# Kernel optimization log

Measured on AMD Instinct MI355X. Metric: run time of the kernel, lower is better.

The kernel has to match this reference:

```python
import jax, jax.numpy as jnp
import numpy as np

B = 2048; V = 2000; L = 20; E = 300; ENC = 128; DEC = 32; ATT = 128


def setup_inputs() -> dict:
    key = jax.random.key(0)
    ks = jax.random.split(key, 24)

    def lin(k, out_f, in_f, s=0.05):
        k1, k2 = jax.random.split(k)
        return (jax.random.normal(k1, (out_f, in_f), jnp.float32) * s,
                jax.random.normal(k2, (out_f,), jnp.float32) * s)

    d = {}
    d["grid_embedding"] = jax.random.normal(ks[0], (B, 5, 5, E), jnp.float32)
    d["grid_onehot"] = jax.random.uniform(ks[1], (B, 5, 5, 7), jnp.float32)
    d["inventory"] = jax.random.normal(ks[2], (B, 10, E), jnp.float32)
    d["goal"] = jax.random.normal(ks[3], (B, E), jnp.float32)
    d["encoded_captions"] = jax.random.randint(ks[4], (B, L), 0, V)
    d["caption_length"] = L  # uniform lengths -> batch_size_t == B each step
    d["W_embed"], d["b_embed"] = lin(ks[5], ENC, E)
    d["W_onehot"], d["b_onehot"] = lin(ks[6], ENC, 7)
    d["W_inv"], d["b_inv"] = lin(ks[7], ENC, E)
    d["W_goal"], d["b_goal"] = lin(ks[8], ENC, E)
    d["W_enc_att"], d["b_enc_att"] = lin(ks[9], ATT, ENC)
    d["W_dec_att"], d["b_dec_att"] = lin(ks[10], ATT, DEC)
    d["W_full_att"], d["b_full_att"] = lin(ks[11], 1, ATT)
    d["emb_table"] = jax.random.normal(ks[12], (V + 1, E), jnp.float32) * 0.05
    d["W_ih"], d["b_ih"] = lin(ks[13], 4 * DEC, E + ENC)  # PyTorch LSTMCell i,f,g,o
    d["W_hh"], d["b_hh"] = lin(ks[14], 4 * DEC, DEC)
    d["W_init_h"], d["b_init_h"] = lin(ks[15], DEC, ENC)
    d["W_init_c"], d["b_init_c"] = lin(ks[16], DEC, ENC)
    d["W_fbeta"], d["b_fbeta"] = lin(ks[17], ENC, DEC)
    d["W_fc"], d["b_fc"] = lin(ks[18], V, DEC)
    return d


def reference(grid_embedding, grid_onehot, inventory, goal, encoded_captions, caption_length,
              W_embed, b_embed, W_onehot, b_onehot, W_inv, b_inv, W_goal, b_goal,
              W_enc_att, b_enc_att, W_dec_att, b_dec_att, W_full_att, b_full_att,
              emb_table, W_ih, b_ih, W_hh, b_hh, W_init_h, b_init_h, W_init_c, b_init_c,
              W_fbeta, b_fbeta, W_fc, b_fc):
    relu = jax.nn.relu
    sig = jax.nn.sigmoid
    # Encoder: grid (B,5,5,*) -> (B,25,ENC); inventory -> (B,10,ENC); goal -> (B,1,ENC)
    c1 = relu(jnp.einsum('bhwe,ce->bhwc', grid_embedding, W_embed) + b_embed)
    c2 = relu(jnp.einsum('bhws,cs->bhwc', grid_onehot, W_onehot) + b_onehot)
    grid = (c1 + c2).reshape(c1.shape[0], 25, -1)
    c3 = relu(inventory @ W_inv.T + b_inv)
    c4 = relu(goal @ W_goal.T + b_goal)[:, None, :]
    enc = jnp.concatenate([grid, c3, c4], axis=1)  # (B, 36, ENC)

    mean_enc = enc.mean(axis=1)
    h = mean_enc @ W_init_h.T + b_init_h  # (B, DEC)
    c = mean_enc @ W_init_c.T + b_init_c
    att1 = enc @ W_enc_att.T + b_enc_att  # (B, 36, ATT), time-invariant, precomputed

    emb = emb_table[encoded_captions]  # (B, L, E)
    T = caption_length - 1
    xs = jnp.transpose(emb[:, :T, :], (1, 0, 2))  # (T, B, E)

    def step(carry, emb_t):
        h, c = carry
        # additive attention
        att2 = h @ W_dec_att.T + b_dec_att
        e = relu(att1 + att2[:, None, :]) @ W_full_att[0] + b_full_att[0]  # (B, 36)
        alpha = jax.nn.softmax(e, axis=1)
        awe = jnp.einsum('bpe,bp->be', enc, alpha)
        gate = sig(h @ W_fbeta.T + b_fbeta)
        x = jnp.concatenate([emb_t, gate * awe], axis=1)
        # PyTorch LSTMCell
        gates = x @ W_ih.T + b_ih + h @ W_hh.T + b_hh
        i, f, g, o = jnp.split(gates, 4, axis=1)
        c_new = sig(f) * c + sig(i) * jnp.tanh(g)
        h_new = sig(o) * jnp.tanh(c_new)
        preds = h_new @ W_fc.T + b_fc  # dropout is identity at eval
        return (h_new, c_new), (preds, alpha)

    (h, c), (preds, alphas) = jax.lax.scan(step, (h, c), xs)
    predictions = jnp.transpose(preds, (1, 0, 2))  # (B, T, V)
    alphas = jnp.transpose(alphas, (1, 0, 2))      # (B, T, 36)
    return predictions, alphas, h
```

## Files before the change

### kernel.cpp

```cpp
#include <hip/hip_runtime.h>


__device__ __forceinline__ float dot4f(float4 a, float4 b) {
  return fmaf(a.x, b.x, fmaf(a.y, b.y, fmaf(a.z, b.z, a.w * b.w)));
}
__device__ __forceinline__ float sigmf_(float x) {
  x = fminf(fmaxf(x, -30.f), 30.f);
  return 1.f / (1.f + __expf(-x));
}
__device__ __forceinline__ float tanhf_(float x) {
  x = fminf(fmaxf(x, -15.f), 15.f);
  float e = __expf(2.f * x);
  return (e - 1.f) / (e + 1.f);
}

__global__ __launch_bounds__(256, 2) void lin_gemm(
    const float* __restrict__ X, int xstride, const int* __restrict__ gather,
    const float* __restrict__ W, int K, int wstride,
    const float* __restrict__ bias,
    const float* __restrict__ X2, const float* __restrict__ W2,
    const float* __restrict__ bias2,
    float* __restrict__ Y, int omode, int relu) {
  __shared__ __align__(16) float Xs[16 * 260];
  __shared__ __align__(16) float Ws[16 * 132];
  const int tid = threadIdx.x;
  const int tc = tid & 15, tr = tid >> 4;
  const int rbase = blockIdx.x * 256;

  float acc[16][8];
#pragma unroll
  for (int i = 0; i < 16; ++i)
#pragma unroll
    for (int j = 0; j < 8; ++j) acc[i][j] = 0.f;

  for (int k0 = 0; k0 < K; k0 += 16) {
#pragma unroll
    for (int it = 0; it < 4; ++it) {
      int tsk = tid + it * 256;
      int r = tsk >> 2, kq = tsk & 3;
      int rg = rbase + r;
      const float* xrow =
          gather ? (X + (size_t)gather[(rg / 19) * 20 + (rg % 19)] * xstride)
                 : (X + (size_t)rg * xstride);
      int kk = k0 + kq * 4;
      float4 v;
      if (kk + 3 < K)
        v = *(const float4*)(xrow + kk);
      else {
        v.x = (kk + 0 < K) ? xrow[kk + 0] : 0.f;
        v.y = (kk + 1 < K) ? xrow[kk + 1] : 0.f;
        v.z = (kk + 2 < K) ? xrow[kk + 2] : 0.f;
        v.w = (kk + 3 < K) ? xrow[kk + 3] : 0.f;
      }
      Xs[(kq * 4 + 0) * 260 + r] = v.x;
      Xs[(kq * 4 + 1) * 260 + r] = v.y;
      Xs[(kq * 4 + 2) * 260 + r] = v.z;
      Xs[(kq * 4 + 3) * 260 + r] = v.w;
    }
#pragma unroll
    for (int it = 0; it < 2; ++it) {
      int tsk = tid + it * 256;
      int c = tsk >> 2, kq = tsk & 3;
      const float* wrow = W + (size_t)c * wstride;
      int kk = k0 + kq * 4;
      float4 v;
      if (kk + 3 < K)
        v = *(const float4*)(wrow + kk);
      else {
        v.x = (kk + 0 < K) ? wrow[kk + 0] : 0.f;
        v.y = (kk + 1 < K) ? wrow[kk + 1] : 0.f;
        v.z = (kk + 2 < K) ? wrow[kk + 2] : 0.f;
        v.w = (kk + 3 < K) ? wrow[kk + 3] : 0.f;
      }
      Ws[(kq * 4 + 0) * 132 + c] = v.x;
      Ws[(kq * 4 + 1) * 132 + c] = v.y;
      Ws[(kq * 4 + 2) * 132 + c] = v.z;
      Ws[(kq * 4 + 3) * 132 + c] = v.w;
    }
    __syncthreads();
#pragma unroll
    for (int kk = 0; kk < 16; ++kk) {
      const float* xp = &Xs[kk * 260 + tr * 16];
      float4 xa = *(const float4*)(xp);
      float4 xb = *(const float4*)(xp + 4);
      float4 xc = *(const float4*)(xp + 8);
      float4 xd = *(const float4*)(xp + 12);
      float4 wA = *(const float4*)&Ws[kk * 132 + tc * 4];
      float4 wB = *(const float4*)&Ws[kk * 132 + 64 + tc * 4];
      float xr[16] = {xa.x, xa.y, xa.z, xa.w, xb.x, xb.y, xb.z, xb.w,
                      xc.x, xc.y, xc.z, xc.w, xd.x, xd.y, xd.z, xd.w};
      float wr[8] = {wA.x, wA.y, wA.z, wA.w, wB.x, wB.y, wB.z, wB.w};
#pragma unroll
      for (int i = 0; i < 16; ++i)
#pragma unroll
        for (int j = 0; j < 8; ++j) acc[i][j] = fmaf(xr[i], wr[j], acc[i][j]);
    }
    __syncthreads();
  }

  float w2r[7][8];
  if (X2) {
#pragma unroll
    for (int k = 0; k < 7; ++k)
      Xs[k * 260 + tid] = X2[(size_t)(rbase + tid) * 7 + k];
#pragma unroll
    for (int it = 0; it < 4; ++it) {
      int tsk = tid + it * 256;
      int c = tsk >> 3, k = tsk & 7;
      if (k < 7) Ws[k * 132 + c] = W2[(size_t)c * 7 + k];
    }
    __syncthreads();
#pragma unroll
    for (int k = 0; k < 7; ++k) {
      float4 a = *(const float4*)&Ws[k * 132 + tc * 4];
      float4 b = *(const float4*)&Ws[k * 132 + 64 + tc * 4];
      w2r[k][0] = a.x; w2r[k][1] = a.y; w2r[k][2] = a.z; w2r[k][3] = a.w;
      w2r[k][4] = b.x; w2r[k][5] = b.y; w2r[k][6] = b.z; w2r[k][7] = b.w;
    }
  }

  float4 bA = *(const float4*)(bias + tc * 4);
  float4 bB = *(const float4*)(bias + 64 + tc * 4);
  float bq[8] = {bA.x, bA.y, bA.z, bA.w, bB.x, bB.y, bB.z, bB.w};
  float b2q[8];
  if (X2) {
    float4 cA = *(const float4*)(bias2 + tc * 4);
    float4 cB = *(const float4*)(bias2 + 64 + tc * 4);
    b2q[0] = cA.x; b2q[1] = cA.y; b2q[2] = cA.z; b2q[3] = cA.w;
    b2q[4] = cB.x; b2q[5] = cB.y; b2q[6] = cB.z; b2q[7] = cB.w;
  }

#pragma unroll
  for (int i = 0; i < 16; ++i) {
    int rg = rbase + tr * 16 + i;
    size_t orow;
    if (omode == 0)
      orow = (size_t)((rg / 25) * 36 + rg % 25) * 128;
    else if (omode == 1)
      orow = (size_t)((rg / 10) * 36 + 25 + rg % 10) * 128;
    else if (omode == 2)
      orow = (size_t)rg * 36 * 128 + 35 * 128;
    else
      orow = (size_t)rg * 128;
    float o[8];
#pragma unroll
    for (int j = 0; j < 8; ++j) {
      float v = acc[i][j] + bq[j];
      if (relu) v = fmaxf(v, 0.f);
      o[j] = v;
    }
    if (X2) {
      float a2[8];
#pragma unroll
      for (int j = 0; j < 8; ++j) a2[j] = b2q[j];
#pragma unroll
      for (int k = 0; k < 7; ++k) {
        float xv = Xs[k * 260 + tr * 16 + i];
#pragma unroll
        for (int j = 0; j < 8; ++j) a2[j] = fmaf(xv, w2r[k][j], a2[j]);
      }
#pragma unroll
      for (int j = 0; j < 8; ++j) o[j] += fmaxf(a2[j], 0.f);
    }
    *(float4*)(Y + orow + tc * 4) = make_float4(o[0], o[1], o[2], o[3]);
    *(float4*)(Y + orow + 64 + tc * 4) = make_float4(o[4], o[5], o[6], o[7]);
  }
}

__global__ void init_hc(const float* __restrict__ enc,
                        const float* __restrict__ Wh, const float* __restrict__ bh,
                        const float* __restrict__ Wc, const float* __restrict__ bc,
                        float* __restrict__ h0, float* __restrict__ c0) {
  int b = blockIdx.x, l = threadIdx.x;
  __shared__ __align__(16) float mean[128];
  float s0 = 0.f, s1 = 0.f;
  const float* e = enc + (size_t)b * 36 * 128;
  for (int p = 0; p < 36; ++p) {
    s0 += e[p * 128 + l];
    s1 += e[p * 128 + 64 + l];
  }
  mean[l] = s0 * (1.f / 36.f);
  mean[64 + l] = s1 * (1.f / 36.f);
  __syncthreads();
  int k = l & 31;
  const float* Wm = (l < 32) ? Wh : Wc;
  float a = (l < 32) ? bh[k] : bc[k];
#pragma unroll
  for (int c4 = 0; c4 < 32; ++c4) {
    float4 mq = *(const float4*)&mean[c4 * 4];
    float4 wv = *(const float4*)(Wm + (size_t)k * 128 + c4 * 4);
    a += dot4f(mq, wv);
  }
  if (l < 32)
    h0[(size_t)b * 32 + k] = a;
  else
    c0[(size_t)b * 32 + k] = a;
}

#define SLOT(w, r) (18944 + (((w) * 3 + ((r) < (w) ? (r) : (r) - 1)) << 7))

__global__ __launch_bounds__(256, 2) void recurrent_k(
    const float* __restrict__ ws_enc, const float* __restrict__ ws_att1,
    const float* __restrict__ ws_embW, const float* __restrict__ ws_h0,
    const float* __restrict__ ws_c0, const float* __restrict__ W_dec_att,
    const float* __restrict__ b_dec_att, const float* __restrict__ W_full_att,
    const float* __restrict__ W_ih, const float* __restrict__ W_hh,
    const float* __restrict__ b_hh, const float* __restrict__ W_fbeta,
    const float* __restrict__ b_fbeta, float* __restrict__ ws_H,
    float* __restrict__ out_alpha, float* __restrict__ out_h) {
  extern __shared__ float lds[];
  const int tid = threadIdx.x;
  const int wave = tid >> 6, lane = tid & 63;
  const int m = lane & 31, s = lane >> 5;
  const int b = blockIdx.x * 4 + wave;

  const int encB = wave * 4608;
  const int x2B = 18432 + wave * 128;
  const int att2B = SLOT((wave + 1) & 3, wave);
  const int ghB = SLOT((wave + 2) & 3, wave);

  float a1m[64];
  {
    const float* base = ws_att1 + ((size_t)b * 36 + m) * 128 + 64 * s;
#pragma unroll
    for (int q4 = 0; q4 < 16; ++q4) {
      float4 v = *(const float4*)(base + 4 * q4);
      a1m[4 * q4 + 0] = v.x; a1m[4 * q4 + 1] = v.y;
      a1m[4 * q4 + 2] = v.z; a1m[4 * q4 + 3] = v.w;
    }
  }
  float a1x[8];
  {
    const float* base =
        ws_att1 + ((size_t)b * 36 + 32 + (lane & 3)) * 128 + (lane >> 2) * 8;
    float4 v0 = *(const float4*)(base);
    float4 v1 = *(const float4*)(base + 4);
    a1x[0] = v0.x; a1x[1] = v0.y; a1x[2] = v0.z; a1x[3] = v0.w;
    a1x[4] = v1.x; a1x[5] = v1.y; a1x[6] = v1.z; a1x[7] = v1.w;
  }
  float wq[4][16];
#pragma unroll
  for (int j = 0; j < 4; ++j) {
    const float* base =
        W_ih + (size_t)(4 * m + j) * 428 + 300 + 32 * wave + 16 * s;
#pragma unroll
    for (int qq = 0; qq < 4; ++qq) {
      float4 v = *(const float4*)(base + 4 * qq);
      wq[j][4 * qq + 0] = v.x; wq[j][4 * qq + 1] = v.y;
      wq[j][4 * qq + 2] = v.z; wq[j][4 * qq + 3] = v.w;
    }
  }
  const float bdec0 = b_dec_att[lane], bdec1 = b_dec_att[lane + 64];
  float4 bfbq = *(const float4*)(b_fbeta + 4 * m);
  float4 bhhq = *(const float4*)(b_hh + 4 * m);
  float creg[4];
  {
    float4 cq = *(const float4*)(ws_c0 + (size_t)b * 32 + 4 * (m & 7));
    creg[0] = cq.x; creg[1] = cq.y; creg[2] = cq.z; creg[3] = cq.w;
  }

  {
    const float* src = ws_enc + (size_t)blockIdx.x * 4 * 4608;
    for (int i = tid; i < 4608; i += 256)
      *(float4*)&lds[i * 4] = *(const float4*)(src + (size_t)i * 4);
  }
  if (m < 8 && s == 0) {
    float4 hq = *(const float4*)(ws_h0 + (size_t)b * 32 + 4 * m);
    *(float4*)&lds[ghB + 4 * m] = hq;
  }
  __syncthreads();

  for (int t = 0; t < 19; ++t) {
    float at2a = bdec0, at2b = bdec1;
    float whhp0 = 0, whhp1 = 0, whhp2 = 0, whhp3 = 0;
    float gatp0 = 0, gatp1 = 0, gatp2 = 0, gatp3 = 0;
#pragma unroll
    for (int kc = 0; kc < 8; ++kc) {
      float4 hq = *(const float4*)&lds[ghB + kc * 4];
      float4 wa = *(const float4*)(W_dec_att + (size_t)lane * 32 + kc * 4);
      float4 wb = *(const float4*)(W_dec_att + (size_t)(lane + 64) * 32 + kc * 4);
      at2a += dot4f(hq, wa);
      at2b += dot4f(hq, wb);
      if ((kc >> 2) == s) {
        float4 w0 = *(const float4*)(W_hh + (size_t)(4 * m + 0) * 32 + kc * 4);
        float4 w1 = *(const float4*)(W_hh + (size_t)(4 * m + 1) * 32 + kc * 4);
        float4 w2 = *(const float4*)(W_hh + (size_t)(4 * m + 2) * 32 + kc * 4);
        float4 w3 = *(const float4*)(W_hh + (size_t)(4 * m + 3) * 32 + kc * 4);
        whhp0 += dot4f(hq, w0); whhp1 += dot4f(hq, w1);
        whhp2 += dot4f(hq, w2); whhp3 += dot4f(hq, w3);
        float4 f0 = *(const float4*)(W_fbeta + (size_t)(4 * m + 0) * 32 + kc * 4);
        float4 f1 = *(const float4*)(W_fbeta + (size_t)(4 * m + 1) * 32 + kc * 4);
        float4 f2 = *(const float4*)(W_fbeta + (size_t)(4 * m + 2) * 32 + kc * 4);
        float4 f3 = *(const float4*)(W_fbeta + (size_t)(4 * m + 3) * 32 + kc * 4);
        gatp0 += dot4f(hq, f0); gatp1 += dot4f(hq, f1);
        gatp2 += dot4f(hq, f2); gatp3 += dot4f(hq, f3);
      }
    }
    lds[att2B + lane] = at2a;
    lds[att2B + 64 + lane] = at2b;

    float ep = 0.f;
#pragma unroll
    for (int q4 = 0; q4 < 16; ++q4) {
      float4 a2v = *(const float4*)&lds[att2B + 64 * s + 4 * q4];
      float4 wfv = *(const float4*)(W_full_att + 64 * s + 4 * q4);
      ep += fmaxf(a1m[4 * q4 + 0] + a2v.x, 0.f) * wfv.x;
      ep += fmaxf(a1m[4 * q4 + 1] + a2v.y, 0.f) * wfv.y;
      ep += fmaxf(a1m[4 * q4 + 2] + a2v.z, 0.f) * wfv.z;
      ep += fmaxf(a1m[4 * q4 + 3] + a2v.w, 0.f) * wfv.w;
    }
    ep += __shfl_xor(ep, 32);
    float ex2 = 0.f;
    {
      int a0 = (lane >> 2) * 8;
      float4 xa = *(const float4*)&lds[att2B + a0];
      float4 xb = *(const float4*)&lds[att2B + a0 + 4];
      float4 fa = *(const float4*)(W_full_att + a0);
      float4 fb = *(const float4*)(W_full_att + a0 + 4);
      ex2 += fmaxf(a1x[0] + xa.x, 0.f) * fa.x;
      ex2 += fmaxf(a1x[1] + xa.y, 0.f) * fa.y;
      ex2 += fmaxf(a1x[2] + xa.z, 0.f) * fa.z;
      ex2 += fmaxf(a1x[3] + xa.w, 0.f) * fa.w;
      ex2 += fmaxf(a1x[4] + xb.x, 0.f) * fb.x;
      ex2 += fmaxf(a1x[5] + xb.y, 0.f) * fb.y;
      ex2 += fmaxf(a1x[6] + xb.z, 0.f) * fb.z;
      ex2 += fmaxf(a1x[7] + xb.w, 0.f) * fb.w;
      ex2 += __shfl_xor(ex2, 4);
      ex2 += __shfl_xor(ex2, 8);
      ex2 += __shfl_xor(ex2, 16);
      ex2 += __shfl_xor(ex2, 32);
    }
    float ev = (s == 0) ? ep : ((m < 4) ? ex2 : -1e30f);
    float mx = ev;
    mx = fmaxf(mx, __shfl_xor(mx, 1));
    mx = fmaxf(mx, __shfl_xor(mx, 2));
    mx = fmaxf(mx, __shfl_xor(mx, 4));
    mx = fmaxf(mx, __shfl_xor(mx, 8));
    mx = fmaxf(mx, __shfl_xor(mx, 16));
    mx = fmaxf(mx, __shfl_xor(mx, 32));
    float eu = __expf(ev - mx);
    float su = eu;
    su += __shfl_xor(su, 1);
    su += __shfl_xor(su, 2);
    su += __shfl_xor(su, 4);
    su += __shfl_xor(su, 8);
    su += __shfl_xor(su, 16);
    su += __shfl_xor(su, 32);
    float alpha = eu / su;
    {
      size_t ob = ((size_t)b * 19 + t) * 36;
      if (s == 0)
        out_alpha[ob + m] = alpha;
      else if (m < 4)
        out_alpha[ob + 32 + m] = alpha;
    }

    float aw0 = 0, aw1 = 0, aw2 = 0, aw3 = 0;
#pragma unroll
    for (int pp = 0; pp < 18; ++pp) {
      float al = __shfl(alpha, 18 * s + pp);
      float4 evv = *(const float4*)&lds[encB + (18 * s + pp) * 128 + 4 * m];
      aw0 += evv.x * al; aw1 += evv.y * al;
      aw2 += evv.z * al; aw3 += evv.w * al;
    }
    aw0 += __shfl_xor(aw0, 32); aw1 += __shfl_xor(aw1, 32);
    aw2 += __shfl_xor(aw2, 32); aw3 += __shfl_xor(aw3, 32);

    float g0 = gatp0 + __shfl_xor(gatp0, 32) + bfbq.x;
    float g1 = gatp1 + __shfl_xor(gatp1, 32) + bfbq.y;
    float g2 = gatp2 + __shfl_xor(gatp2, 32) + bfbq.z;
    float g3 = gatp3 + __shfl_xor(gatp3, 32) + bfbq.w;
    float x20 = sigmf_(g0) * aw0, x21 = sigmf_(g1) * aw1;
    float x22 = sigmf_(g2) * aw2, x23 = sigmf_(g3) * aw3;
    if (s == 0) *(float4*)&lds[x2B + 4 * m] = make_float4(x20, x21, x22, x23);
    __syncthreads();

    float ownE0 = 0, ownE1 = 0, ownE2 = 0, ownE3 = 0;
#pragma unroll
    for (int rr = 0; rr < 4; ++rr) {
      float p0 = 0, p1 = 0, p2 = 0, p3 = 0;
#pragma unroll
      for (int cc = 0; cc < 4; ++cc) {
        float4 xv = *(const float4*)&lds[18432 + rr * 128 + 32 * wave + 16 * s + 4 * cc];
        p0 += wq[0][4 * cc + 0] * xv.x + wq[0][4 * cc + 1] * xv.y +
              wq[0][4 * cc + 2] * xv.z + wq[0][4 * cc + 3] * xv.w;
        p1 += wq[1][4 * cc + 0] * xv.x + wq[1][4 * cc + 1] * xv.y +
              wq[1][4 * cc + 2] * xv.z + wq[1][4 * cc + 3] * xv.w;
        p2 += wq[2][4 * cc + 0] * xv.x + wq[2][4 * cc + 1] * xv.y +
              wq[2][4 * cc + 2] * xv.z + wq[2][4 * cc + 3] * xv.w;
        p3 += wq[3][4 * cc + 0] * xv.x + wq[3][4 * cc + 1] * xv.y +
              wq[3][4 * cc + 2] * xv.z + wq[3][4 * cc + 3] * xv.w;
      }
      if (rr == wave) {
        ownE0 = p0; ownE1 = p1; ownE2 = p2; ownE3 = p3;
      } else {
        p0 += __shfl_xor(p0, 32); p1 += __shfl_xor(p1, 32);
        p2 += __shfl_xor(p2, 32); p3 += __shfl_xor(p3, 32);
        if (s == 0)
          *(float4*)&lds[SLOT(wave, rr) + 4 * m] = make_float4(p0, p1, p2, p3);
      }
    }
    __syncthreads();

    float own0 = ownE0 + whhp0, own1 = ownE1 + whhp1;
    float own2 = ownE2 + whhp2, own3 = ownE3 + whhp3;
    own0 += __shfl_xor(own0, 32); own1 += __shfl_xor(own1, 32);
    own2 += __shfl_xor(own2, 32); own3 += __shfl_xor(own3, 32);
    float4 fA = *(const float4*)&lds[SLOT((wave + 1) & 3, wave) + 4 * m];
    float4 fB = *(const float4*)&lds[SLOT((wave + 2) & 3, wave) + 4 * m];
    float4 fC = *(const float4*)&lds[SLOT((wave + 3) & 3, wave) + 4 * m];
    float4 ew = *(const float4*)(ws_embW + ((size_t)b * 19 + t) * 128 + 4 * m);
    float gg0 = own0 + fA.x + fB.x + fC.x + ew.x + bhhq.x;
    float gg1 = own1 + fA.y + fB.y + fC.y + ew.y + bhhq.y;
    float gg2 = own2 + fA.z + fB.z + fC.z + ew.z + bhhq.z;
    float gg3 = own3 + fA.w + fB.w + fC.w + ew.w + bhhq.w;
    if (s == 0) *(float4*)&lds[ghB + 4 * m] = make_float4(gg0, gg1, gg2, gg3);
    if (m < 8) {
      float4 gi = *(const float4*)&lds[ghB + 4 * m];
      float4 gf = *(const float4*)&lds[ghB + 32 + 4 * m];
      float4 gG = *(const float4*)&lds[ghB + 64 + 4 * m];
      float4 go = *(const float4*)&lds[ghB + 96 + 4 * m];
      float c0n = sigmf_(gf.x) * creg[0] + sigmf_(gi.x) * tanhf_(gG.x);
      float c1n = sigmf_(gf.y) * creg[1] + sigmf_(gi.y) * tanhf_(gG.y);
      float c2n = sigmf_(gf.z) * creg[2] + sigmf_(gi.z) * tanhf_(gG.z);
      float c3n = sigmf_(gf.w) * creg[3] + sigmf_(gi.w) * tanhf_(gG.w);
      float h0n = sigmf_(go.x) * tanhf_(c0n);
      float h1n = sigmf_(go.y) * tanhf_(c1n);
      float h2n = sigmf_(go.z) * tanhf_(c2n);
      float h3n = sigmf_(go.w) * tanhf_(c3n);
      creg[0] = c0n; creg[1] = c1n; creg[2] = c2n; creg[3] = c3n;
      if (s == 0) {
        float4 hv = make_float4(h0n, h1n, h2n, h3n);
        *(float4*)&lds[ghB + 4 * m] = hv;
        *(float4*)(ws_H + ((size_t)b * 19 + t) * 32 + 4 * m) = hv;
        if (t == 18) *(float4*)(out_h + (size_t)b * 32 + 4 * m) = hv;
      }
    }
  }
}

#define FC_RB 152
#define FC_WT_ST 1026
#define FC_HS_ST 154

__global__ __launch_bounds__(512, 1) void fc_out2(const float* __restrict__ H,
                                                  const float* __restrict__ W,
                                                  const float* __restrict__ bias,
                                                  float* __restrict__ Y) {
  extern __shared__ float sm[];
  float* Wt = sm;
  float* Hs = sm + 32 * FC_WT_ST;
  const int tid = threadIdx.x;
  const int tc = tid & 127;
  const int rt = tid >> 7;
  const int rbase = blockIdx.x * FC_RB;

  for (int i = tid; i < FC_RB * 8; i += 512) {
    int r = i >> 3, kq = i & 7;
    float4 v = *(const float4*)(H + (size_t)(rbase + r) * 32 + kq * 4);
    Hs[(kq * 4 + 0) * FC_HS_ST + r] = v.x;
    Hs[(kq * 4 + 1) * FC_HS_ST + r] = v.y;
    Hs[(kq * 4 + 2) * FC_HS_ST + r] = v.z;
    Hs[(kq * 4 + 3) * FC_HS_ST + r] = v.w;
  }

  for (int ph = 0; ph < 2; ++ph) {
    const int phbase = ph * 1024;
    const int ncols = (ph == 0) ? 1024 : 976;
    __syncthreads();
    for (int c = tid; c < ncols; c += 512) {
      const float* wrow = W + (size_t)(phbase + c) * 32;
#pragma unroll
      for (int q = 0; q < 8; ++q) {
        float4 v = *(const float4*)(wrow + q * 4);
        Wt[(q * 4 + 0) * FC_WT_ST + c] = v.x;
        Wt[(q * 4 + 1) * FC_WT_ST + c] = v.y;
        Wt[(q * 4 + 2) * FC_WT_ST + c] = v.z;
        Wt[(q * 4 + 3) * FC_WT_ST + c] = v.w;
      }
    }
    __syncthreads();

    float bq[4][2];
#pragma unroll
    for (int ch = 0; ch < 4; ++ch) {
      int col = phbase + ch * 256 + 2 * tc;
      bq[ch][0] = (col < 2000) ? bias[col] : 0.f;
      bq[ch][1] = (col < 2000) ? bias[col + 1] : 0.f;
    }

    for (int pass = 0; pass < 5; ++pass) {
      int r0 = pass * 32 + rt * 8;
      if (r0 + 8 > FC_RB) continue;
      float acc[8][8];
#pragma unroll
      for (int i = 0; i < 8; ++i)
#pragma unroll
        for (int j = 0; j < 8; ++j) acc[i][j] = 0.f;
#pragma unroll 8
      for (int k = 0; k < 32; ++k) {
        float4 ha = *(const float4*)&Hs[k * FC_HS_ST + r0];
        float4 hb = *(const float4*)&Hs[k * FC_HS_ST + r0 + 4];
        float hr[8] = {ha.x, ha.y, ha.z, ha.w, hb.x, hb.y, hb.z, hb.w};
        float2 w0 = *(const float2*)&Wt[k * FC_WT_ST + 0 * 256 + 2 * tc];
        float2 w1 = *(const float2*)&Wt[k * FC_WT_ST + 1 * 256 + 2 * tc];
        float2 w2 = *(const float2*)&Wt[k * FC_WT_ST + 2 * 256 + 2 * tc];
        float2 w3 = *(const float2*)&Wt[k * FC_WT_ST + 3 * 256 + 2 * tc];
        float wc[8] = {w0.x, w0.y, w1.x, w1.y, w2.x, w2.y, w3.x, w3.y};
#pragma unroll
        for (int i = 0; i < 8; ++i)
#pragma unroll
          for (int j = 0; j < 8; ++j) acc[i][j] = fmaf(hr[i], wc[j], acc[i][j]);
      }
#pragma unroll
      for (int i = 0; i < 8; ++i) {
        size_t row = (size_t)(rbase + r0 + i);
#pragma unroll
        for (int ch = 0; ch < 4; ++ch) {
          int col = phbase + ch * 256 + 2 * tc;
          if (col < 2000) {
            float2 v;
            v.x = acc[i][2 * ch + 0] + bq[ch][0];
            v.y = acc[i][2 * ch + 1] + bq[ch][1];
            *(float2*)(Y + row * 2000 + col) = v;
          }
        }
      }
    }
  }
}

extern "C" void kernel_launch(void* const* d_in, const int* in_sizes, int n_in,
                              void* d_out, int out_size, void* d_ws,
                              size_t ws_size, hipStream_t stream) {
  (void)in_sizes; (void)n_in; (void)out_size; (void)ws_size;
  const float* grid_embedding = (const float*)d_in[0];
  const float* grid_onehot = (const float*)d_in[1];
  const float* inventory = (const float*)d_in[2];
  const float* goal = (const float*)d_in[3];
  const int* captions = (const int*)d_in[4];
  const float* W_embed = (const float*)d_in[6];
  const float* b_embed = (const float*)d_in[7];
  const float* W_onehot = (const float*)d_in[8];
  const float* b_onehot = (const float*)d_in[9];
  const float* W_inv = (const float*)d_in[10];
  const float* b_inv = (const float*)d_in[11];
  const float* W_goal = (const float*)d_in[12];
  const float* b_goal = (const float*)d_in[13];
  const float* W_enc_att = (const float*)d_in[14];
  const float* b_enc_att = (const float*)d_in[15];
  const float* W_dec_att = (const float*)d_in[16];
  const float* b_dec_att = (const float*)d_in[17];
  const float* W_full_att = (const float*)d_in[18];
  const float* emb_table = (const float*)d_in[20];
  const float* W_ih = (const float*)d_in[21];
  const float* b_ih = (const float*)d_in[22];
  const float* W_hh = (const float*)d_in[23];
  const float* b_hh = (const float*)d_in[24];
  const float* W_init_h = (const float*)d_in[25];
  const float* b_init_h = (const float*)d_in[26];
  const float* W_init_c = (const float*)d_in[27];
  const float* b_init_c = (const float*)d_in[28];
  const float* W_fbeta = (const float*)d_in[29];
  const float* b_fbeta = (const float*)d_in[30];
  const float* W_fc = (const float*)d_in[31];
  const float* b_fc = (const float*)d_in[32];

  float* out = (float*)d_out;
  float* preds = out;
  float* alphas = out + (size_t)77824000;
  float* houtp = out + (size_t)79224832;

  float* ws = (float*)d_ws;
  float* ws_enc = ws;
  float* ws_att1 = ws_enc + (size_t)9437184;
  float* ws_embW = ws_att1 + (size_t)9437184;
  float* ws_H = ws_embW + (size_t)4980736;
  float* ws_h0 = ws_H + (size_t)1245184;
  float* ws_c0 = ws_h0 + (size_t)65536;

  lin_gemm<<<200, 256, 0, stream>>>(grid_embedding, 300, nullptr, W_embed, 300,
                                    300, b_embed, grid_onehot, W_onehot,
                                    b_onehot, ws_enc, 0, 1);
  lin_gemm<<<80, 256, 0, stream>>>(inventory, 300, nullptr, W_inv, 300, 300,
                                   b_inv, nullptr, nullptr, nullptr, ws_enc, 1, 1);
  lin_gemm<<<8, 256, 0, stream>>>(goal, 300, nullptr, W_goal, 300, 300, b_goal,
                                  nullptr, nullptr, nullptr, ws_enc, 2, 1);
  init_hc<<<2048, 64, 0, stream>>>(ws_enc, W_init_h, b_init_h, W_init_c,
                                   b_init_c, ws_h0, ws_c0);
  lin_gemm<<<288, 256, 0, stream>>>(ws_enc, 128, nullptr, W_enc_att, 128, 128,
                                    b_enc_att, nullptr, nullptr, nullptr,
                                    ws_att1, 3, 0);
  lin_gemm<<<152, 256, 0, stream>>>(emb_table, 300, captions, W_ih, 300, 428,
                                    b_ih, nullptr, nullptr, nullptr, ws_embW, 3, 0);
  hipFuncSetAttribute((const void*)recurrent_k,
                      hipFuncAttributeMaxDynamicSharedMemorySize, 81920);
  recurrent_k<<<512, 256, 81920, stream>>>(
      ws_enc, ws_att1, ws_embW, ws_h0, ws_c0, W_dec_att, b_dec_att, W_full_att,
      W_ih, W_hh, b_hh, W_fbeta, b_fbeta, ws_H, alphas, houtp);
  hipFuncSetAttribute((const void*)fc_out2,
                      hipFuncAttributeMaxDynamicSharedMemorySize, 151040);
  fc_out2<<<256, 512, 151040, stream>>>(ws_H, W_fc, b_fc, preds);
}
```

Measured before the change: 1.627 ms.

## Stage recurrent weights in LDS transposed and keep encoder rows in registers

The recurrent kernel now copies W_dec_att, W_hh, W_fbeta (transposed) and W_full_att into LDS once, instead of re-reading them from global memory on every time step. Each lane keeps its two encoder columns across all 36 positions in registers (float2 x36), so the attention-weighted sum runs without LDS encoder reads or cross-half shuffles. The per-step embW load is issued at the top of the loop to hide its latency. LDS use drops from 80KB to about 57KB, but register pressure grows with 72 extra floats per lane, which could cause spills under launch_bounds(256,2).

```diff
diff --git a/kernel.cpp b/kernel.cpp
--- a/kernel.cpp
+++ b/kernel.cpp
@@ -197,7 +197,11 @@
     c0[(size_t)b * 32 + k] = a;
 }
 
-#define SLOT(w, r) (18944 + (((w) * 3 + ((r) < (w) ? (r) : (r) - 1)) << 7))
+#define RK_WHH 4096
+#define RK_WFB 8192
+#define RK_WFA 12288
+#define RK_X2 12416
+#define SLOT(w, r) (12928 + (((w) * 3 + ((r) < (w) ? (r) : (r) - 1)) << 7))
 
 __global__ __launch_bounds__(256, 2) void recurrent_k(
     const float* __restrict__ ws_enc, const float* __restrict__ ws_att1,
@@ -214,11 +218,36 @@
   const int m = lane & 31, s = lane >> 5;
   const int b = blockIdx.x * 4 + wave;
 
-  const int encB = wave * 4608;
-  const int x2B = 18432 + wave * 128;
+  const int x2B = RK_X2 + wave * 128;
   const int att2B = SLOT((wave + 1) & 3, wave);
   const int ghB = SLOT((wave + 2) & 3, wave);
 
+  for (int tsk = tid; tsk < 1024; tsk += 256) {
+    int row = tsk & 127, kq = tsk >> 7;
+    float4 vd = *(const float4*)(W_dec_att + (size_t)row * 32 + kq * 4);
+    lds[(4 * kq + 0) * 128 + row] = vd.x;
+    lds[(4 * kq + 1) * 128 + row] = vd.y;
+    lds[(4 * kq + 2) * 128 + row] = vd.z;
+    lds[(4 * kq + 3) * 128 + row] = vd.w;
+    float4 vh = *(const float4*)(W_hh + (size_t)row * 32 + kq * 4);
+    lds[RK_WHH + (4 * kq + 0) * 128 + row] = vh.x;
+    lds[RK_WHH + (4 * kq + 1) * 128 + row] = vh.y;
+    lds[RK_WHH + (4 * kq + 2) * 128 + row] = vh.z;
+    lds[RK_WHH + (4 * kq + 3) * 128 + row] = vh.w;
+    float4 vf = *(const float4*)(W_fbeta + (size_t)row * 32 + kq * 4);
+    lds[RK_WFB + (4 * kq + 0) * 128 + row] = vf.x;
+    lds[RK_WFB + (4 * kq + 1) * 128 + row] = vf.y;
+    lds[RK_WFB + (4 * kq + 2) * 128 + row] = vf.z;
+    lds[RK_WFB + (4 * kq + 3) * 128 + row] = vf.w;
+  }
+  if (tid < 128) lds[RK_WFA + tid] = W_full_att[tid];
+
+  float2 enc_r[36];
+  {
+    const float* ebase = ws_enc + (size_t)b * 4608 + 2 * lane;
+#pragma unroll
+    for (int p = 0; p < 36; ++p) enc_r[p] = *(const float2*)(ebase + p * 128);
+  }
   float a1m[64];
   {
     const float* base = ws_att1 + ((size_t)b * 36 + m) * 128 + 64 * s;
@@ -251,19 +280,13 @@
     }
   }
   const float bdec0 = b_dec_att[lane], bdec1 = b_dec_att[lane + 64];
-  float4 bfbq = *(const float4*)(b_fbeta + 4 * m);
+  const float2 bfb2 = *(const float2*)(b_fbeta + 2 * lane);
   float4 bhhq = *(const float4*)(b_hh + 4 * m);
   float creg[4];
   {
     float4 cq = *(const float4*)(ws_c0 + (size_t)b * 32 + 4 * (m & 7));
     creg[0] = cq.x; creg[1] = cq.y; creg[2] = cq.z; creg[3] = cq.w;
   }
-
-  {
-    const float* src = ws_enc + (size_t)blockIdx.x * 4 * 4608;
-    for (int i = tid; i < 4608; i += 256)
-      *(float4*)&lds[i * 4] = *(const float4*)(src + (size_t)i * 4);
-  }
   if (m < 8 && s == 0) {
     float4 hq = *(const float4*)(ws_h0 + (size_t)b * 32 + 4 * m);
     *(float4*)&lds[ghB + 4 * m] = hq;
@@ -271,30 +294,27 @@
   __syncthreads();
 
   for (int t = 0; t < 19; ++t) {
+    float4 ew = *(const float4*)(ws_embW + ((size_t)b * 19 + t) * 128 + 4 * m);
+
     float at2a = bdec0, at2b = bdec1;
+    float ga = 0.f, gb = 0.f;
+#pragma unroll
+    for (int k = 0; k < 32; ++k) {
+      float hk = lds[ghB + k];
+      at2a = fmaf(hk, lds[k * 128 + lane], at2a);
+      at2b = fmaf(hk, lds[k * 128 + 64 + lane], at2b);
+      float2 wf = *(const float2*)&lds[RK_WFB + k * 128 + 2 * lane];
+      ga = fmaf(hk, wf.x, ga);
+      gb = fmaf(hk, wf.y, gb);
+    }
     float whhp0 = 0, whhp1 = 0, whhp2 = 0, whhp3 = 0;
-    float gatp0 = 0, gatp1 = 0, gatp2 = 0, gatp3 = 0;
-#pragma unroll
-    for (int kc = 0; kc < 8; ++kc) {
-      float4 hq = *(const float4*)&lds[ghB + kc * 4];
-      float4 wa = *(const float4*)(W_dec_att + (size_t)lane * 32 + kc * 4);
-      float4 wb = *(const float4*)(W_dec_att + (size_t)(lane + 64) * 32 + kc * 4);
-      at2a += dot4f(hq, wa);
-      at2b += dot4f(hq, wb);
-      if ((kc >> 2) == s) {
-        float4 w0 = *(const float4*)(W_hh + (size_t)(4 * m + 0) * 32 + kc * 4);
-        float4 w1 = *(const float4*)(W_hh + (size_t)(4 * m + 1) * 32 + kc * 4);
-        float4 w2 = *(const float4*)(W_hh + (size_t)(4 * m + 2) * 32 + kc * 4);
-        float4 w3 = *(const float4*)(W_hh + (size_t)(4 * m + 3) * 32 + kc * 4);
-        whhp0 += dot4f(hq, w0); whhp1 += dot4f(hq, w1);
-        whhp2 += dot4f(hq, w2); whhp3 += dot4f(hq, w3);
-        float4 f0 = *(const float4*)(W_fbeta + (size_t)(4 * m + 0) * 32 + kc * 4);
-        float4 f1 = *(const float4*)(W_fbeta + (size_t)(4 * m + 1) * 32 + kc * 4);
-        float4 f2 = *(const float4*)(W_fbeta + (size_t)(4 * m + 2) * 32 + kc * 4);
-        float4 f3 = *(const float4*)(W_fbeta + (size_t)(4 * m + 3) * 32 + kc * 4);
-        gatp0 += dot4f(hq, f0); gatp1 += dot4f(hq, f1);
-        gatp2 += dot4f(hq, f2); gatp3 += dot4f(hq, f3);
-      }
+#pragma unroll
+    for (int kc = 0; kc < 16; ++kc) {
+      int k = 16 * s + kc;
+      float hk = lds[ghB + k];
+      float4 wh = *(const float4*)&lds[RK_WHH + k * 128 + 4 * m];
+      whhp0 = fmaf(hk, wh.x, whhp0); whhp1 = fmaf(hk, wh.y, whhp1);
+      whhp2 = fmaf(hk, wh.z, whhp2); whhp3 = fmaf(hk, wh.w, whhp3);
     }
     lds[att2B + lane] = at2a;
     lds[att2B + 64 + lane] = at2b;
@@ -303,7 +323,7 @@
 #pragma unroll
     for (int q4 = 0; q4 < 16; ++q4) {
       float4 a2v = *(const float4*)&lds[att2B + 64 * s + 4 * q4];
-      float4 wfv = *(const float4*)(W_full_att + 64 * s + 4 * q4);
+      float4 wfv = *(const float4*)&lds[RK_WFA + 64 * s + 4 * q4];
       ep += fmaxf(a1m[4 * q4 + 0] + a2v.x, 0.f) * wfv.x;
       ep += fmaxf(a1m[4 * q4 + 1] + a2v.y, 0.f) * wfv.y;
       ep += fmaxf(a1m[4 * q4 + 2] + a2v.z, 0.f) * wfv.z;
@@ -315,8 +335,8 @@
       int a0 = (lane >> 2) * 8;
       float4 xa = *(const float4*)&lds[att2B + a0];
       float4 xb = *(const float4*)&lds[att2B + a0 + 4];
-      float4 fa = *(const float4*)(W_full_att + a0);
-      float4 fb = *(const float4*)(W_full_att + a0 + 4);
+      float4 fa = *(const float4*)&lds[RK_WFA + a0];
+      float4 fb = *(const float4*)&lds[RK_WFA + a0 + 4];
       ex2 += fmaxf(a1x[0] + xa.x, 0.f) * fa.x;
       ex2 += fmaxf(a1x[1] + xa.y, 0.f) * fa.y;
       ex2 += fmaxf(a1x[2] + xa.z, 0.f) * fa.z;
@@ -355,24 +375,17 @@
         out_alpha[ob + 32 + m] = alpha;
     }
 
-    float aw0 = 0, aw1 = 0, aw2 = 0, aw3 = 0;
-#pragma unroll
-    for (int pp = 0; pp < 18; ++pp) {
-      float al = __shfl(alpha, 18 * s + pp);
-      float4 evv = *(const float4*)&lds[encB + (18 * s + pp) * 128 + 4 * m];
-      aw0 += evv.x * al; aw1 += evv.y * al;
-      aw2 += evv.z * al; aw3 += evv.w * al;
-    }
-    aw0 += __shfl_xor(aw0, 32); aw1 += __shfl_xor(aw1, 32);
-    aw2 += __shfl_xor(aw2, 32); aw3 += __shfl_xor(aw3, 32);
-
-    float g0 = gatp0 + __shfl_xor(gatp0, 32) + bfbq.x;
-    float g1 = gatp1 + __shfl_xor(gatp1, 32) + bfbq.y;
-    float g2 = gatp2 + __shfl_xor(gatp2, 32) + bfbq.z;
-    float g3 = gatp3 + __shfl_xor(gatp3, 32) + bfbq.w;
-    float x20 = sigmf_(g0) * aw0, x21 = sigmf_(g1) * aw1;
-    float x22 = sigmf_(g2) * aw2, x23 = sigmf_(g3) * aw3;
-    if (s == 0) *(float4*)&lds[x2B + 4 * m] = make_float4(x20, x21, x22, x23);
+    float aw0 = 0.f, aw1 = 0.f;
+#pragma unroll
+    for (int p = 0; p < 36; ++p) {
+      float al = __shfl(alpha, p);
+      aw0 = fmaf(enc_r[p].x, al, aw0);
+      aw1 = fmaf(enc_r[p].y, al, aw1);
+    }
+
+    float x2a = sigmf_(ga + bfb2.x) * aw0;
+    float x2b = sigmf_(gb + bfb2.y) * aw1;
+    *(float2*)&lds[x2B + 2 * lane] = make_float2(x2a, x2b);
     __syncthreads();
 
     float ownE0 = 0, ownE1 = 0, ownE2 = 0, ownE3 = 0;
@@ -381,7 +394,8 @@
       float p0 = 0, p1 = 0, p2 = 0, p3 = 0;
 #pragma unroll
       for (int cc = 0; cc < 4; ++cc) {
-        float4 xv = *(const float4*)&lds[18432 + rr * 128 + 32 * wave + 16 * s + 4 * cc];
+        float4 xv =
+            *(const float4*)&lds[RK_X2 + rr * 128 + 32 * wave + 16 * s + 4 * cc];
         p0 += wq[0][4 * cc + 0] * xv.x + wq[0][4 * cc + 1] * xv.y +
               wq[0][4 * cc + 2] * xv.z + wq[0][4 * cc + 3] * xv.w;
         p1 += wq[1][4 * cc + 0] * xv.x + wq[1][4 * cc + 1] * xv.y +
@@ -409,7 +423,6 @@
     float4 fA = *(const float4*)&lds[SLOT((wave + 1) & 3, wave) + 4 * m];
     float4 fB = *(const float4*)&lds[SLOT((wave + 2) & 3, wave) + 4 * m];
     float4 fC = *(const float4*)&lds[SLOT((wave + 3) & 3, wave) + 4 * m];
-    float4 ew = *(const float4*)(ws_embW + ((size_t)b * 19 + t) * 128 + 4 * m);
     float gg0 = own0 + fA.x + fB.x + fC.x + ew.x + bhhq.x;
     float gg1 = own1 + fA.y + fB.y + fC.y + ew.y + bhhq.y;
     float gg2 = own2 + fA.z + fB.z + fC.z + ew.z + bhhq.z;
@@ -594,8 +607,8 @@
   lin_gemm<<<152, 256, 0, stream>>>(emb_table, 300, captions, W_ih, 300, 428,
                                     b_ih, nullptr, nullptr, nullptr, ws_embW, 3, 0);
   hipFuncSetAttribute((const void*)recurrent_k,
-                      hipFuncAttributeMaxDynamicSharedMemorySize, 81920);
-  recurrent_k<<<512, 256, 81920, stream>>>(
+                      hipFuncAttributeMaxDynamicSharedMemorySize, 57856);
+  recurrent_k<<<512, 256, 57856, stream>>>(
       ws_enc, ws_att1, ws_embW, ws_h0, ws_c0, W_dec_att, b_dec_att, W_full_att,
       W_ih, W_hh, b_hh, W_fbeta, b_fbeta, ws_H, alphas, houtp);
   hipFuncSetAttribute((const void*)fc_out2,
```

New measurement: 1.996 ms. 22.6% more time.
